# Kernel tuning notes

Hardware: AMD Instinct MI355X
Metric: run time of the kernel (lower is better)

Reference implementation:

```python
import jax, jax.numpy as jnp
import numpy as np

NUM_HEADS = 16
ROPE_BASE = 10000.0

def _rope(x):
    # x: (B, T, H, hd), rotate-half 1D RoPE over temporal axis
    B, T, H, hd = x.shape
    inv_freq = 1.0 / (ROPE_BASE ** (jnp.arange(0, hd, 2, dtype=jnp.float32) / hd))  # (hd/2,)
    freqs = jnp.arange(T, dtype=jnp.float32)[:, None] * inv_freq[None, :]            # (T, hd/2)
    emb = jnp.concatenate([freqs, freqs], axis=-1)                                    # (T, hd)
    cos = jnp.cos(emb)[None, :, None, :]
    sin = jnp.sin(emb)[None, :, None, :]
    x1, x2 = jnp.split(x, 2, axis=-1)
    rot = jnp.concatenate([-x2, x1], axis=-1)
    return x * cos + rot * sin

def setup_inputs() -> dict:
    key = jax.random.key(0)
    ks = jax.random.split(key, 7)
    B, T, S, D = 4, 16, 256, 2048
    std = 0.02
    return {
        'v_p': jax.random.normal(ks[0], (B, T, S, D), jnp.float32),
        'v_f': jax.random.normal(ks[1], (B, T, S, D), jnp.float32),
        'a_p': jax.random.normal(ks[2], (B, T, D), jnp.float32),
        'a_f': jax.random.normal(ks[3], (B, T, D), jnp.float32),
        'W_qkv': jax.random.normal(ks[4], (D, 3 * D), jnp.float32) * std,
        'W_proj': jax.random.normal(ks[5], (D, D), jnp.float32) * std,
        'b_proj': jnp.zeros((D,), jnp.float32),
    }

def reference(v_p, v_f, a_p, a_f, W_qkv, W_proj, b_proj):
    B, T_p, S, D = v_p.shape
    T_f = v_f.shape[1]
    H = NUM_HEADS
    hd = D // H
    scale = hd ** -0.5
    # pool spatial dim and concatenate streams: [v_p, v_f, a_p, a_f]
    tokens = jnp.concatenate([v_p.mean(axis=2), v_f.mean(axis=2), a_p, a_f], axis=1)  # (B, T, D)
    T = tokens.shape[1]
    qkv = tokens @ W_qkv  # qkv_bias=False
    q, k, v = jnp.split(qkv, 3, axis=-1)
    q = q.reshape(B, T, H, hd)
    k = k.reshape(B, T, H, hd)
    v = v.reshape(B, T, H, hd)
    q = _rope(q)
    k = _rope(k)
    scores = jnp.einsum('bqhd,bkhd->bhqk', q, k) * scale
    causal_mask = jnp.triu(jnp.ones((T, T), dtype=bool), k=1)
    scores = jnp.where(causal_mask[None, None], -jnp.inf, scores)
    attn = jax.nn.softmax(scores, axis=-1)
    out = jnp.einsum('bhqk,bkhd->bqhd', attn, v).reshape(B, T, D)
    out = out @ W_proj + b_proj
    v_p_out = jnp.broadcast_to(out[:, :T_p, None, :], (B, T_p, S, D))
    v_f_out = jnp.broadcast_to(out[:, T_p:T_p + T_f, None, :], (B, T_f, S, D))
    a_p_out = out[:, T_p + T_f:T_p + T_f + T_p]
    a_f_out = out[:, T_p + T_f + T_p:]
    return (v_p_out, v_f_out, a_p_out, a_f_out)
```

## Files before the change

### kernel.cpp

```cpp
#include <hip/hip_runtime.h>
#include <hip/hip_bf16.h>
#include <stdint.h>


using bf16x8v = __attribute__((ext_vector_type(8))) __bf16;
using f32x4v  = __attribute__((ext_vector_type(4))) float;

union Pack8 { __bf16 h[8]; uint4 u; };
union Pack4 { __bf16 h[4]; uint2 u; };

__device__ __forceinline__ int swz(int r, int c) {
    return (r << 6) + ((c ^ (r & 7)) << 3);
}
__device__ __forceinline__ int aswz(int r, int c) {
    return (r << 7) + ((c ^ (r & 31)) << 2);
}

__global__ __launch_bounds__(256) void prep_mean_kernel(
    const float* __restrict__ v_p, const float* __restrict__ v_f,
    float* __restrict__ partials,
    const float* __restrict__ W_qkv, const float* __restrict__ W_proj,
    __bf16* __restrict__ Wt_qkv, __bf16* __restrict__ Wt_proj)
{
    __shared__ float Ls[64][68];
    int bid0 = blockIdx.x;
    if (bid0 < 2048) {
        int bid = bid0;
        int which  = bid >> 10;
        int rem    = bid & 1023;
        int row    = rem >> 4;
        int dchunk = (rem >> 3) & 1;
        int schunk = rem & 7;
        int d = (dchunk << 10) + (threadIdx.x << 2);
        const float* src = (which ? v_f : v_p) + ((size_t)row << 19)
                         + ((size_t)(schunk << 5) << 11) + d;
        float4 a = {0.f, 0.f, 0.f, 0.f};
        #pragma unroll 8
        for (int s = 0; s < 32; ++s) {
            float4 x = *reinterpret_cast<const float4*>(src + ((size_t)s << 11));
            a.x += x.x; a.y += x.y; a.z += x.z; a.w += x.w;
        }
        int pr = which * 64 + row;
        *reinterpret_cast<float4*>(&partials[(size_t)((pr << 3) + schunk) * 2048 + d]) = a;
    } else {
        int bid = bid0 - 2048;
        const float* src; __bf16* dst; int N, tile;
        if (bid < 3072) { src = W_qkv;  dst = Wt_qkv;  N = 6144; tile = bid; }
        else            { src = W_proj; dst = Wt_proj; N = 2048; tile = bid - 3072; }
        int tiles_n = N >> 6;
        int tn = tile % tiles_n;
        int tk = tile / tiles_n;
        int t = threadIdx.x;
        int rb = t >> 4;
        int c4 = (t & 15) << 2;
        #pragma unroll
        for (int s = 0; s < 4; ++s) {
            int r = rb + (s << 4);
            float4 v = *reinterpret_cast<const float4*>(
                src + (size_t)(tk * 64 + r) * N + tn * 64 + c4);
            *reinterpret_cast<float4*>(&Ls[r][c4]) = v;
        }
        __syncthreads();
        int c  = t >> 2;
        int r0 = (t & 3) << 4;
        Pack8 p0, p1;
        #pragma unroll
        for (int i = 0; i < 8; ++i) p0.h[i] = (__bf16)Ls[r0 + i][c];
        #pragma unroll
        for (int i = 0; i < 8; ++i) p1.h[i] = (__bf16)Ls[r0 + 8 + i][c];
        __bf16* drow = dst + (size_t)(tn * 64 + c) * 2048 + tk * 64 + r0;
        *reinterpret_cast<uint4*>(drow)     = p0.u;
        *reinterpret_cast<uint4*>(drow + 8) = p1.u;
    }
}

__global__ __launch_bounds__(256) void tokens_finish_kernel(
    const float* __restrict__ partials, const float* __restrict__ a_p,
    const float* __restrict__ a_f, __bf16* __restrict__ tokens_bf)
{
    int bid = blockIdx.x;
    if (bid < 128) {
        int idx = (bid * 256 + threadIdx.x) * 8;
        int r = idx >> 11;
        int d = idx & 2047;
        float s[8];
        #pragma unroll
        for (int i = 0; i < 8; ++i) s[i] = 0.f;
        #pragma unroll
        for (int sc = 0; sc < 8; ++sc) {
            const float* p = partials + (size_t)((r << 3) + sc) * 2048 + d;
            float4 x0 = *reinterpret_cast<const float4*>(p);
            float4 x1 = *reinterpret_cast<const float4*>(p + 4);
            s[0] += x0.x; s[1] += x0.y; s[2] += x0.z; s[3] += x0.w;
            s[4] += x1.x; s[5] += x1.y; s[6] += x1.z; s[7] += x1.w;
        }
        const float inv = 1.f / 256.f;
        int which = r >> 6, rr = r & 63;
        int b = rr >> 4, tt = rr & 15;
        int tokrow = b * 64 + which * 16 + tt;
        Pack8 p;
        #pragma unroll
        for (int i = 0; i < 8; ++i) p.h[i] = (__bf16)(s[i] * inv);
        *reinterpret_cast<uint4*>(&tokens_bf[(size_t)tokrow * 2048 + d]) = p.u;
    } else {
        int g = (bid - 128) * 256 + threadIdx.x;
        int which = g >> 14;
        int j = g & 16383;
        int b = j >> 12;
        int rr = j & 4095;
        int tt = rr >> 8;
        int gq = rr & 255;
        const float* src = (which ? a_f : a_p) + (size_t)(b * 16 + tt) * 2048 + gq * 8;
        float4 x0 = *reinterpret_cast<const float4*>(src);
        float4 x1 = *reinterpret_cast<const float4*>(src + 4);
        Pack8 p;
        p.h[0] = (__bf16)x0.x; p.h[1] = (__bf16)x0.y; p.h[2] = (__bf16)x0.z; p.h[3] = (__bf16)x0.w;
        p.h[4] = (__bf16)x1.x; p.h[5] = (__bf16)x1.y; p.h[6] = (__bf16)x1.z; p.h[7] = (__bf16)x1.w;
        int tokrow = b * 64 + 32 + which * 16 + tt;
        *reinterpret_cast<uint4*>(&tokens_bf[(size_t)tokrow * 2048 + gq * 8]) = p.u;
    }
}

__global__ __launch_bounds__(256) void gemm_bf16_kernel(
    const __bf16* __restrict__ A, const __bf16* __restrict__ Bt,
    float* __restrict__ C, int N)
{
    __shared__ __bf16 As[4096];
    __shared__ __bf16 Bs[4096];
    const int t = threadIdx.x;
    const int m0 = blockIdx.y << 6;
    const int n0 = blockIdx.x << 6;
    const int kz = blockIdx.z;
    const int kbase = kz << 10;
    const int lane = t & 63;
    const int w = t >> 6;
    const int wm = w << 4;
    const int lrow = lane & 15;
    const int lk = lane >> 4;
    const int srl = lane >> 3;
    const int schunk = lane & 7;

    f32x4v acc[4] = {{0.f,0.f,0.f,0.f},{0.f,0.f,0.f,0.f},
                     {0.f,0.f,0.f,0.f},{0.f,0.f,0.f,0.f}};

    int row_c0 = (w << 4) + srl;
    int row_c1 = row_c0 + 8;
    const __bf16* gA0 = A  + (size_t)(m0 + row_c0) * 2048 + kbase + ((schunk ^ (row_c0 & 7)) << 3);
    const __bf16* gA1 = A  + (size_t)(m0 + row_c1) * 2048 + kbase + ((schunk ^ (row_c1 & 7)) << 3);
    const __bf16* gB0 = Bt + (size_t)(n0 + row_c0) * 2048 + kbase + ((schunk ^ (row_c0 & 7)) << 3);
    const __bf16* gB1 = Bt + (size_t)(n0 + row_c1) * 2048 + kbase + ((schunk ^ (row_c1 & 7)) << 3);
    __bf16* lA0 = &As[(w << 4) << 6];
    __bf16* lA1 = &As[((w << 4) + 8) << 6];
    __bf16* lB0 = &Bs[(w << 4) << 6];
    __bf16* lB1 = &Bs[((w << 4) + 8) << 6];

    for (int kt = 0; kt < 16; ++kt) {
        __syncthreads();
        int ko = kt << 6;
        __builtin_amdgcn_global_load_lds(
            (const __attribute__((address_space(1))) void*)(gA0 + ko),
            (__attribute__((address_space(3))) void*)lA0, 16, 0, 0);
        __builtin_amdgcn_global_load_lds(
            (const __attribute__((address_space(1))) void*)(gA1 + ko),
            (__attribute__((address_space(3))) void*)lA1, 16, 0, 0);
        __builtin_amdgcn_global_load_lds(
            (const __attribute__((address_space(1))) void*)(gB0 + ko),
            (__attribute__((address_space(3))) void*)lB0, 16, 0, 0);
        __builtin_amdgcn_global_load_lds(
            (const __attribute__((address_space(1))) void*)(gB1 + ko),
            (__attribute__((address_space(3))) void*)lB1, 16, 0, 0);
        __syncthreads();
        #pragma unroll
        for (int s = 0; s < 2; ++s) {
            int cA = (s << 2) + lk;
            bf16x8v af = *reinterpret_cast<const bf16x8v*>(&As[swz(wm + lrow, cA)]);
            #pragma unroll
            for (int j = 0; j < 4; ++j) {
                bf16x8v bf = *reinterpret_cast<const bf16x8v*>(&Bs[swz((j << 4) + lrow, cA)]);
                acc[j] = __builtin_amdgcn_mfma_f32_16x16x32_bf16(af, bf, acc[j], 0, 0, 0);
            }
        }
    }
    float* Cz = C + (size_t)kz * 256 * N;
    #pragma unroll
    for (int j = 0; j < 4; ++j) {
        int col = n0 + (j << 4) + lrow;
        #pragma unroll
        for (int e = 0; e < 4; ++e) {
            int row = m0 + wm + (lk << 2) + e;
            Cz[(size_t)row * N + col] = acc[j][e];
        }
    }
}

__global__ __launch_bounds__(256) void attn_kernel(
    const float* __restrict__ qkv, __bf16* __restrict__ attn_out)
{
    __shared__ float q_s[64 * 128];
    __shared__ float k_s[64 * 128];
    const size_t PART = (size_t)256 * 6144;
    int b = blockIdx.x >> 4;
    int h = blockIdx.x & 15;
    int tid = threadIdx.x;
    const float* base0 = qkv + (size_t)(b * 64) * 6144 + h * 128;
    const float* base1 = base0 + PART;
    const float L2C = 0.20762050593046012f;
    #pragma unroll
    for (int r = 0; r < 4; ++r) {
        int idx = tid + (r << 8);
        int tq = idx >> 4;
        int cg = idx & 15;
        int d = cg << 2;
        const float* s0 = base0 + (size_t)tq * 6144;
        const float* s1 = base1 + (size_t)tq * 6144;
        float4 q1a = *reinterpret_cast<const float4*>(s0 + d);
        float4 q1b = *reinterpret_cast<const float4*>(s1 + d);
        float4 q2a = *reinterpret_cast<const float4*>(s0 + d + 64);
        float4 q2b = *reinterpret_cast<const float4*>(s1 + d + 64);
        float4 k1a = *reinterpret_cast<const float4*>(s0 + 2048 + d);
        float4 k1b = *reinterpret_cast<const float4*>(s1 + 2048 + d);
        float4 k2a = *reinterpret_cast<const float4*>(s0 + 2048 + d + 64);
        float4 k2b = *reinterpret_cast<const float4*>(s1 + 2048 + d + 64);
        float4 q1 = {q1a.x + q1b.x, q1a.y + q1b.y, q1a.z + q1b.z, q1a.w + q1b.w};
        float4 q2 = {q2a.x + q2b.x, q2a.y + q2b.y, q2a.z + q2b.z, q2a.w + q2b.w};
        float4 k1 = {k1a.x + k1b.x, k1a.y + k1b.y, k1a.z + k1b.z, k1a.w + k1b.w};
        float4 k2 = {k2a.x + k2b.x, k2a.y + k2b.y, k2a.z + k2b.z, k2a.w + k2b.w};
        float ft = (float)tq;
        float a0 = ft * exp2f(-(float)(d + 0) * L2C);
        float a1 = ft * exp2f(-(float)(d + 1) * L2C);
        float a2 = ft * exp2f(-(float)(d + 2) * L2C);
        float a3 = ft * exp2f(-(float)(d + 3) * L2C);
        float c0 = cosf(a0), s0f = sinf(a0);
        float c1 = cosf(a1), s1f = sinf(a1);
        float c2 = cosf(a2), s2f = sinf(a2);
        float c3 = cosf(a3), s3f = sinf(a3);
        float4 qa, qb, ka, kb;
        qa.x = q1.x * c0 - q2.x * s0f;  qb.x = q2.x * c0 + q1.x * s0f;
        qa.y = q1.y * c1 - q2.y * s1f;  qb.y = q2.y * c1 + q1.y * s1f;
        qa.z = q1.z * c2 - q2.z * s2f;  qb.z = q2.z * c2 + q1.z * s2f;
        qa.w = q1.w * c3 - q2.w * s3f;  qb.w = q2.w * c3 + q1.w * s3f;
        ka.x = k1.x * c0 - k2.x * s0f;  kb.x = k2.x * c0 + k1.x * s0f;
        ka.y = k1.y * c1 - k2.y * s1f;  kb.y = k2.y * c1 + k1.y * s1f;
        ka.z = k1.z * c2 - k2.z * s2f;  kb.z = k2.z * c2 + k1.z * s2f;
        ka.w = k1.w * c3 - k2.w * s3f;  kb.w = k2.w * c3 + k1.w * s3f;
        *reinterpret_cast<float4*>(&q_s[aswz(tq, cg)])      = qa;
        *reinterpret_cast<float4*>(&q_s[aswz(tq, cg + 16)]) = qb;
        *reinterpret_cast<float4*>(&k_s[aswz(tq, cg)])      = ka;
        *reinterpret_cast<float4*>(&k_s[aswz(tq, cg + 16)]) = kb;
    }
    __syncthreads();
    int qi = tid >> 2;
    int g  = tid & 3;
    float pv[16];
    #pragma unroll
    for (int j = 0; j < 16; ++j) pv[j] = 0.f;
    for (int c = 0; c < 32; ++c) {
        float4 a = *reinterpret_cast<const float4*>(&q_s[aswz(qi, c)]);
        #pragma unroll
        for (int j = 0; j < 16; ++j) {
            int ki = (j << 2) + g;
            float4 bb = *reinterpret_cast<const float4*>(&k_s[aswz(ki, c)]);
            pv[j] += a.x * bb.x + a.y * bb.y + a.z * bb.z + a.w * bb.w;
        }
    }
    const float scale = 0.0883883476483184405f;
    float m = -1e30f;
    #pragma unroll
    for (int j = 0; j < 16; ++j) {
        int ki = (j << 2) + g;
        pv[j] = (ki <= qi) ? pv[j] * scale : -1e30f;
        m = fmaxf(m, pv[j]);
    }
    m = fmaxf(m, __shfl_xor(m, 1));
    m = fmaxf(m, __shfl_xor(m, 2));
    float l = 0.f;
    #pragma unroll
    for (int j = 0; j < 16; ++j) {
        float e = (pv[j] > -1e29f) ? expf(pv[j] - m) : 0.f;
        pv[j] = e;
        l += e;
    }
    l += __shfl_xor(l, 1);
    l += __shfl_xor(l, 2);
    float inv_l = 1.f / l;
    __syncthreads();
    float* p_s = q_s;
    #pragma unroll
    for (int j = 0; j < 16; ++j) p_s[qi * 65 + (j << 2) + g] = pv[j] * inv_l;
    float* v_s = k_s;
    #pragma unroll
    for (int r = 0; r < 8; ++r) {
        int idx = tid + (r << 8);
        int tv = idx >> 5;
        int c = idx & 31;
        float4 va = *reinterpret_cast<const float4*>(base0 + (size_t)tv * 6144 + 4096 + (c << 2));
        float4 vb = *reinterpret_cast<const float4*>(base1 + (size_t)tv * 6144 + 4096 + (c << 2));
        float4 vs = {va.x + vb.x, va.y + vb.y, va.z + vb.z, va.w + vb.w};
        *reinterpret_cast<float4*>(&v_s[aswz(tv, c)]) = vs;
    }
    __syncthreads();
    float4 acc[8];
    #pragma unroll
    for (int u = 0; u < 8; ++u) acc[u] = {0.f, 0.f, 0.f, 0.f};
    for (int ki = 0; ki < 64; ++ki) {
        float p = p_s[qi * 65 + ki];
        #pragma unroll
        for (int u = 0; u < 8; ++u) {
            float4 vv = *reinterpret_cast<const float4*>(&v_s[aswz(ki, g + (u << 2))]);
            acc[u].x += p * vv.x;
            acc[u].y += p * vv.y;
            acc[u].z += p * vv.z;
            acc[u].w += p * vv.w;
        }
    }
    __bf16* orow = attn_out + (size_t)(b * 64 + qi) * 2048 + h * 128 + (g << 2);
    #pragma unroll
    for (int u = 0; u < 8; ++u) {
        Pack4 p4;
        p4.h[0] = (__bf16)acc[u].x; p4.h[1] = (__bf16)acc[u].y;
        p4.h[2] = (__bf16)acc[u].z; p4.h[3] = (__bf16)acc[u].w;
        *reinterpret_cast<uint2*>(orow + (u << 4)) = p4.u;
    }
}

__global__ __launch_bounds__(256) void outputs_kernel(
    const float* __restrict__ outp, const float* __restrict__ b_proj,
    float* __restrict__ d_out)
{
    const size_t PART = (size_t)256 * 2048;
    int bid = blockIdx.x;
    if (bid < 2048) {
        int which = bid >> 10;
        int rem = bid & 1023;
        int row = rem >> 4;
        int schunk = rem & 15;
        int b = row >> 4;
        int t = row & 15;
        size_t srcoff = (size_t)(b * 64 + (which << 4) + t) * 2048 + threadIdx.x * 8;
        const float* s0 = outp + srcoff;
        const float* s1 = outp + PART + srcoff;
        float4 a0 = *reinterpret_cast<const float4*>(s0);
        float4 a1 = *reinterpret_cast<const float4*>(s0 + 4);
        float4 b0 = *reinterpret_cast<const float4*>(s1);
        float4 b1 = *reinterpret_cast<const float4*>(s1 + 4);
        float4 v0 = *reinterpret_cast<const float4*>(b_proj + threadIdx.x * 8);
        float4 v1 = *reinterpret_cast<const float4*>(b_proj + threadIdx.x * 8 + 4);
        float4 o0 = {a0.x + b0.x + v0.x, a0.y + b0.y + v0.y,
                     a0.z + b0.z + v0.z, a0.w + b0.w + v0.w};
        float4 o1 = {a1.x + b1.x + v1.x, a1.y + b1.y + v1.y,
                     a1.z + b1.z + v1.z, a1.w + b1.w + v1.w};
        size_t base = (size_t)which * 33554432 +
                      ((size_t)row * 256 + (size_t)schunk * 16) * 2048 + threadIdx.x * 8;
        float* dst = d_out + base;
        #pragma unroll
        for (int s = 0; s < 16; ++s) {
            *reinterpret_cast<float4*>(dst + (size_t)s * 2048)     = o0;
            *reinterpret_cast<float4*>(dst + (size_t)s * 2048 + 4) = o1;
        }
    } else {
        int g8 = (bid - 2048) * 256 + threadIdx.x;
        int which = g8 >> 14;
        int j = g8 & 16383;
        int b = j >> 12;
        int rr = j & 4095;
        int tt = rr >> 8;
        int gq = rr & 255;
        size_t srcoff = (size_t)(b * 64 + 32 + (which << 4) + tt) * 2048 + gq * 8;
        const float* s0 = outp + srcoff;
        const float* s1 = outp + PART + srcoff;
        float4 a0 = *reinterpret_cast<const float4*>(s0);
        float4 a1 = *reinterpret_cast<const float4*>(s0 + 4);
        float4 b0 = *reinterpret_cast<const float4*>(s1);
        float4 b1 = *reinterpret_cast<const float4*>(s1 + 4);
        float4 v0 = *reinterpret_cast<const float4*>(b_proj + gq * 8);
        float4 v1 = *reinterpret_cast<const float4*>(b_proj + gq * 8 + 4);
        float4 x0 = {a0.x + b0.x + v0.x, a0.y + b0.y + v0.y,
                     a0.z + b0.z + v0.z, a0.w + b0.w + v0.w};
        float4 x1 = {a1.x + b1.x + v1.x, a1.y + b1.y + v1.y,
                     a1.z + b1.z + v1.z, a1.w + b1.w + v1.w};
        float* dst = d_out + 67108864 + (size_t)which * 131072 +
                     (size_t)(b * 16 + tt) * 2048 + gq * 8;
        *reinterpret_cast<float4*>(dst)     = x0;
        *reinterpret_cast<float4*>(dst + 4) = x1;
    }
}

extern "C" void kernel_launch(void* const* d_in, const int* in_sizes, int n_in,
                              void* d_out, int out_size, void* d_ws, size_t ws_size,
                              hipStream_t stream)
{
    const float* v_p    = (const float*)d_in[0];
    const float* v_f    = (const float*)d_in[1];
    const float* a_p    = (const float*)d_in[2];
    const float* a_f    = (const float*)d_in[3];
    const float* W_qkv  = (const float*)d_in[4];
    const float* W_proj = (const float*)d_in[5];
    const float* b_proj = (const float*)d_in[6];
    float* out_f = (float*)d_out;

    char* ws = (char*)d_ws;
    __bf16* tokens_bf = (__bf16*)(ws);
    __bf16* Wt_qkv    = (__bf16*)(ws + 1048576);
    __bf16* Wt_proj   = (__bf16*)(ws + 26214400);
    float*  qkv       = (float*)(ws + 34603008);
    __bf16* attn_bf   = (__bf16*)(ws + 47185920);
    float*  outp      = (float*)(ws + 48234496);
    float*  partials  = (float*)(ws + 52428800);

    prep_mean_kernel<<<6144, 256, 0, stream>>>(v_p, v_f, partials,
                                               W_qkv, W_proj, Wt_qkv, Wt_proj);
    tokens_finish_kernel<<<256, 256, 0, stream>>>(partials, a_p, a_f, tokens_bf);
    gemm_bf16_kernel<<<dim3(96, 4, 2), 256, 0, stream>>>(tokens_bf, Wt_qkv, qkv, 6144);
    attn_kernel<<<64, 256, 0, stream>>>(qkv, attn_bf);
    gemm_bf16_kernel<<<dim3(32, 4, 2), 256, 0, stream>>>(attn_bf, Wt_proj, outp, 2048);
    outputs_kernel<<<2176, 256, 0, stream>>>(outp, b_proj, out_f);
}
```

Before: 203.5 us.

## Split attention by query tile with causal K/V trimming; widen output broadcast grid

The attention kernel now launches one block per (batch, head, 16-row query tile) instead of one per (batch, head), and loads and processes only the keys and values up to the causal limit of each tile. This spreads the work over four times as many blocks and skips the masked K/V work, at the cost of recomputing the K RoPE for overlapping rows across tiles. The output broadcast kernel writes 8 spatial rows per block instead of 16, doubling its grid, and the mean-reduction loop unroll goes from 8 to 16.

```diff
diff --git a/kernel.cpp b/kernel.cpp
--- a/kernel.cpp
+++ b/kernel.cpp
@@ -35,7 +35,7 @@
         const float* src = (which ? v_f : v_p) + ((size_t)row << 19)
                          + ((size_t)(schunk << 5) << 11) + d;
         float4 a = {0.f, 0.f, 0.f, 0.f};
-        #pragma unroll 8
+        #pragma unroll 16
         for (int s = 0; s < 32; ++s) {
             float4 x = *reinterpret_cast<const float4*>(src + ((size_t)s << 11));
             a.x += x.x; a.y += x.y; a.z += x.z; a.w += x.w;
@@ -196,36 +196,35 @@
 __global__ __launch_bounds__(256) void attn_kernel(
     const float* __restrict__ qkv, __bf16* __restrict__ attn_out)
 {
-    __shared__ float q_s[64 * 128];
+    __shared__ float q_s[16 * 128];
     __shared__ float k_s[64 * 128];
     const size_t PART = (size_t)256 * 6144;
-    int b = blockIdx.x >> 4;
-    int h = blockIdx.x & 15;
+    int bid = blockIdx.x;
+    int qt = bid & 3;
+    int h  = (bid >> 2) & 15;
+    int b  = bid >> 6;
     int tid = threadIdx.x;
+    int qr0 = qt << 4;
+    int kcap = qr0 + 16;
     const float* base0 = qkv + (size_t)(b * 64) * 6144 + h * 128;
     const float* base1 = base0 + PART;
     const float L2C = 0.20762050593046012f;
-    #pragma unroll
-    for (int r = 0; r < 4; ++r) {
-        int idx = tid + (r << 8);
-        int tq = idx >> 4;
-        int cg = idx & 15;
+    const float scale = 0.0883883476483184405f;
+
+    {
+        int tq = tid >> 4;
+        int cg = tid & 15;
         int d = cg << 2;
-        const float* s0 = base0 + (size_t)tq * 6144;
-        const float* s1 = base1 + (size_t)tq * 6144;
+        int grow = qr0 + tq;
+        const float* s0 = base0 + (size_t)grow * 6144;
+        const float* s1 = base1 + (size_t)grow * 6144;
         float4 q1a = *reinterpret_cast<const float4*>(s0 + d);
         float4 q1b = *reinterpret_cast<const float4*>(s1 + d);
         float4 q2a = *reinterpret_cast<const float4*>(s0 + d + 64);
         float4 q2b = *reinterpret_cast<const float4*>(s1 + d + 64);
-        float4 k1a = *reinterpret_cast<const float4*>(s0 + 2048 + d);
-        float4 k1b = *reinterpret_cast<const float4*>(s1 + 2048 + d);
-        float4 k2a = *reinterpret_cast<const float4*>(s0 + 2048 + d + 64);
-        float4 k2b = *reinterpret_cast<const float4*>(s1 + 2048 + d + 64);
         float4 q1 = {q1a.x + q1b.x, q1a.y + q1b.y, q1a.z + q1b.z, q1a.w + q1b.w};
         float4 q2 = {q2a.x + q2b.x, q2a.y + q2b.y, q2a.z + q2b.z, q2a.w + q2b.w};
-        float4 k1 = {k1a.x + k1b.x, k1a.y + k1b.y, k1a.z + k1b.z, k1a.w + k1b.w};
-        float4 k2 = {k2a.x + k2b.x, k2a.y + k2b.y, k2a.z + k2b.z, k2a.w + k2b.w};
-        float ft = (float)tq;
+        float ft = (float)grow;
         float a0 = ft * exp2f(-(float)(d + 0) * L2C);
         float a1 = ft * exp2f(-(float)(d + 1) * L2C);
         float a2 = ft * exp2f(-(float)(d + 2) * L2C);
@@ -234,92 +233,129 @@
         float c1 = cosf(a1), s1f = sinf(a1);
         float c2 = cosf(a2), s2f = sinf(a2);
         float c3 = cosf(a3), s3f = sinf(a3);
-        float4 qa, qb, ka, kb;
+        float4 qa, qb;
         qa.x = q1.x * c0 - q2.x * s0f;  qb.x = q2.x * c0 + q1.x * s0f;
         qa.y = q1.y * c1 - q2.y * s1f;  qb.y = q2.y * c1 + q1.y * s1f;
         qa.z = q1.z * c2 - q2.z * s2f;  qb.z = q2.z * c2 + q1.z * s2f;
         qa.w = q1.w * c3 - q2.w * s3f;  qb.w = q2.w * c3 + q1.w * s3f;
-        ka.x = k1.x * c0 - k2.x * s0f;  kb.x = k2.x * c0 + k1.x * s0f;
-        ka.y = k1.y * c1 - k2.y * s1f;  kb.y = k2.y * c1 + k1.y * s1f;
-        ka.z = k1.z * c2 - k2.z * s2f;  kb.z = k2.z * c2 + k1.z * s2f;
-        ka.w = k1.w * c3 - k2.w * s3f;  kb.w = k2.w * c3 + k1.w * s3f;
         *reinterpret_cast<float4*>(&q_s[aswz(tq, cg)])      = qa;
         *reinterpret_cast<float4*>(&q_s[aswz(tq, cg + 16)]) = qb;
-        *reinterpret_cast<float4*>(&k_s[aswz(tq, cg)])      = ka;
-        *reinterpret_cast<float4*>(&k_s[aswz(tq, cg + 16)]) = kb;
+    }
+    #pragma unroll
+    for (int r = 0; r < 4; ++r) {
+        int idx = tid + (r << 8);
+        if (idx < (kcap << 4)) {
+            int tk = idx >> 4;
+            int cg = idx & 15;
+            int d = cg << 2;
+            const float* s0 = base0 + (size_t)tk * 6144 + 2048;
+            const float* s1 = base1 + (size_t)tk * 6144 + 2048;
+            float4 k1a = *reinterpret_cast<const float4*>(s0 + d);
+            float4 k1b = *reinterpret_cast<const float4*>(s1 + d);
+            float4 k2a = *reinterpret_cast<const float4*>(s0 + d + 64);
+            float4 k2b = *reinterpret_cast<const float4*>(s1 + d + 64);
+            float4 k1 = {k1a.x + k1b.x, k1a.y + k1b.y, k1a.z + k1b.z, k1a.w + k1b.w};
+            float4 k2 = {k2a.x + k2b.x, k2a.y + k2b.y, k2a.z + k2b.z, k2a.w + k2b.w};
+            float ft = (float)tk;
+            float a0 = ft * exp2f(-(float)(d + 0) * L2C);
+            float a1 = ft * exp2f(-(float)(d + 1) * L2C);
+            float a2 = ft * exp2f(-(float)(d + 2) * L2C);
+            float a3 = ft * exp2f(-(float)(d + 3) * L2C);
+            float c0 = cosf(a0), s0f = sinf(a0);
+            float c1 = cosf(a1), s1f = sinf(a1);
+            float c2 = cosf(a2), s2f = sinf(a2);
+            float c3 = cosf(a3), s3f = sinf(a3);
+            float4 ka, kb;
+            ka.x = k1.x * c0 - k2.x * s0f;  kb.x = k2.x * c0 + k1.x * s0f;
+            ka.y = k1.y * c1 - k2.y * s1f;  kb.y = k2.y * c1 + k1.y * s1f;
+            ka.z = k1.z * c2 - k2.z * s2f;  kb.z = k2.z * c2 + k1.z * s2f;
+            ka.w = k1.w * c3 - k2.w * s3f;  kb.w = k2.w * c3 + k1.w * s3f;
+            *reinterpret_cast<float4*>(&k_s[aswz(tk, cg)])      = ka;
+            *reinterpret_cast<float4*>(&k_s[aswz(tk, cg + 16)]) = kb;
+        }
     }
     __syncthreads();
-    int qi = tid >> 2;
-    int g  = tid & 3;
-    float pv[16];
-    #pragma unroll
-    for (int j = 0; j < 16; ++j) pv[j] = 0.f;
+    int qi = tid >> 4;
+    int g  = tid & 15;
+    int qg = qr0 + qi;
+    float pv[4] = {0.f, 0.f, 0.f, 0.f};
     for (int c = 0; c < 32; ++c) {
         float4 a = *reinterpret_cast<const float4*>(&q_s[aswz(qi, c)]);
         #pragma unroll
-        for (int j = 0; j < 16; ++j) {
-            int ki = (j << 2) + g;
-            float4 bb = *reinterpret_cast<const float4*>(&k_s[aswz(ki, c)]);
-            pv[j] += a.x * bb.x + a.y * bb.y + a.z * bb.z + a.w * bb.w;
-        }
-    }
-    const float scale = 0.0883883476483184405f;
+        for (int j = 0; j < 4; ++j) {
+            if ((j << 4) < kcap) {
+                int ki = (j << 4) + g;
+                float4 bb = *reinterpret_cast<const float4*>(&k_s[aswz(ki, c)]);
+                pv[j] += a.x * bb.x + a.y * bb.y + a.z * bb.z + a.w * bb.w;
+            }
+        }
+    }
     float m = -1e30f;
     #pragma unroll
-    for (int j = 0; j < 16; ++j) {
-        int ki = (j << 2) + g;
-        pv[j] = (ki <= qi) ? pv[j] * scale : -1e30f;
-        m = fmaxf(m, pv[j]);
+    for (int j = 0; j < 4; ++j) {
+        if ((j << 4) < kcap) {
+            int ki = (j << 4) + g;
+            pv[j] = (ki <= qg) ? pv[j] * scale : -1e30f;
+            m = fmaxf(m, pv[j]);
+        }
     }
     m = fmaxf(m, __shfl_xor(m, 1));
     m = fmaxf(m, __shfl_xor(m, 2));
+    m = fmaxf(m, __shfl_xor(m, 4));
+    m = fmaxf(m, __shfl_xor(m, 8));
     float l = 0.f;
     #pragma unroll
-    for (int j = 0; j < 16; ++j) {
-        float e = (pv[j] > -1e29f) ? expf(pv[j] - m) : 0.f;
-        pv[j] = e;
-        l += e;
+    for (int j = 0; j < 4; ++j) {
+        if ((j << 4) < kcap) {
+            float e = (pv[j] > -1e29f) ? expf(pv[j] - m) : 0.f;
+            pv[j] = e;
+            l += e;
+        }
     }
     l += __shfl_xor(l, 1);
     l += __shfl_xor(l, 2);
+    l += __shfl_xor(l, 4);
+    l += __shfl_xor(l, 8);
     float inv_l = 1.f / l;
     __syncthreads();
     float* p_s = q_s;
     #pragma unroll
-    for (int j = 0; j < 16; ++j) p_s[qi * 65 + (j << 2) + g] = pv[j] * inv_l;
+    for (int j = 0; j < 4; ++j) {
+        if ((j << 4) < kcap) p_s[qi * 65 + (j << 4) + g] = pv[j] * inv_l;
+    }
     float* v_s = k_s;
     #pragma unroll
     for (int r = 0; r < 8; ++r) {
         int idx = tid + (r << 8);
-        int tv = idx >> 5;
-        int c = idx & 31;
-        float4 va = *reinterpret_cast<const float4*>(base0 + (size_t)tv * 6144 + 4096 + (c << 2));
-        float4 vb = *reinterpret_cast<const float4*>(base1 + (size_t)tv * 6144 + 4096 + (c << 2));
-        float4 vs = {va.x + vb.x, va.y + vb.y, va.z + vb.z, va.w + vb.w};
-        *reinterpret_cast<float4*>(&v_s[aswz(tv, c)]) = vs;
+        if (idx < (kcap << 5)) {
+            int tv = idx >> 5;
+            int c = idx & 31;
+            float4 va = *reinterpret_cast<const float4*>(base0 + (size_t)tv * 6144 + 4096 + (c << 2));
+            float4 vb = *reinterpret_cast<const float4*>(base1 + (size_t)tv * 6144 + 4096 + (c << 2));
+            float4 vs = {va.x + vb.x, va.y + vb.y, va.z + vb.z, va.w + vb.w};
+            *reinterpret_cast<float4*>(&v_s[aswz(tv, c)]) = vs;
+        }
     }
     __syncthreads();
-    float4 acc[8];
-    #pragma unroll
-    for (int u = 0; u < 8; ++u) acc[u] = {0.f, 0.f, 0.f, 0.f};
-    for (int ki = 0; ki < 64; ++ki) {
+    float4 acc[2] = {{0.f,0.f,0.f,0.f},{0.f,0.f,0.f,0.f}};
+    for (int ki = 0; ki < kcap; ++ki) {
         float p = p_s[qi * 65 + ki];
         #pragma unroll
-        for (int u = 0; u < 8; ++u) {
-            float4 vv = *reinterpret_cast<const float4*>(&v_s[aswz(ki, g + (u << 2))]);
+        for (int u = 0; u < 2; ++u) {
+            float4 vv = *reinterpret_cast<const float4*>(&v_s[aswz(ki, (g << 1) + u)]);
             acc[u].x += p * vv.x;
             acc[u].y += p * vv.y;
             acc[u].z += p * vv.z;
             acc[u].w += p * vv.w;
         }
     }
-    __bf16* orow = attn_out + (size_t)(b * 64 + qi) * 2048 + h * 128 + (g << 2);
-    #pragma unroll
-    for (int u = 0; u < 8; ++u) {
+    __bf16* orow = attn_out + (size_t)(b * 64 + qg) * 2048 + h * 128 + (g << 3);
+    #pragma unroll
+    for (int u = 0; u < 2; ++u) {
         Pack4 p4;
         p4.h[0] = (__bf16)acc[u].x; p4.h[1] = (__bf16)acc[u].y;
         p4.h[2] = (__bf16)acc[u].z; p4.h[3] = (__bf16)acc[u].w;
-        *reinterpret_cast<uint2*>(orow + (u << 4)) = p4.u;
+        *reinterpret_cast<uint2*>(orow + (u << 2)) = p4.u;
     }
 }
 
@@ -329,11 +365,11 @@
 {
     const size_t PART = (size_t)256 * 2048;
     int bid = blockIdx.x;
-    if (bid < 2048) {
-        int which = bid >> 10;
-        int rem = bid & 1023;
-        int row = rem >> 4;
-        int schunk = rem & 15;
+    if (bid < 4096) {
+        int which = bid >> 11;
+        int rem = bid & 2047;
+        int row = rem >> 5;
+        int schunk = rem & 31;
         int b = row >> 4;
         int t = row & 15;
         size_t srcoff = (size_t)(b * 64 + (which << 4) + t) * 2048 + threadIdx.x * 8;
@@ -350,15 +386,15 @@
         float4 o1 = {a1.x + b1.x + v1.x, a1.y + b1.y + v1.y,
                      a1.z + b1.z + v1.z, a1.w + b1.w + v1.w};
         size_t base = (size_t)which * 33554432 +
-                      ((size_t)row * 256 + (size_t)schunk * 16) * 2048 + threadIdx.x * 8;
+                      ((size_t)row * 256 + (size_t)schunk * 8) * 2048 + threadIdx.x * 8;
         float* dst = d_out + base;
         #pragma unroll
-        for (int s = 0; s < 16; ++s) {
+        for (int s = 0; s < 8; ++s) {
             *reinterpret_cast<float4*>(dst + (size_t)s * 2048)     = o0;
             *reinterpret_cast<float4*>(dst + (size_t)s * 2048 + 4) = o1;
         }
     } else {
-        int g8 = (bid - 2048) * 256 + threadIdx.x;
+        int g8 = (bid - 4096) * 256 + threadIdx.x;
         int which = g8 >> 14;
         int j = g8 & 16383;
         int b = j >> 12;
@@ -411,7 +447,7 @@
                                                W_qkv, W_proj, Wt_qkv, Wt_proj);
     tokens_finish_kernel<<<256, 256, 0, stream>>>(partials, a_p, a_f, tokens_bf);
     gemm_bf16_kernel<<<dim3(96, 4, 2), 256, 0, stream>>>(tokens_bf, Wt_qkv, qkv, 6144);
-    attn_kernel<<<64, 256, 0, stream>>>(qkv, attn_bf);
+    attn_kernel<<<256, 256, 0, stream>>>(qkv, attn_bf);
     gemm_bf16_kernel<<<dim3(32, 4, 2), 256, 0, stream>>>(attn_bf, Wt_proj, outp, 2048);
-    outputs_kernel<<<2176, 256, 0, stream>>>(outp, b_proj, out_f);
-}
+    outputs_kernel<<<4224, 256, 0, stream>>>(outp, b_proj, out_f);
+}
```

After: 197.4 us. -3.0%, faster.
